# Kernel tuning notes

Measured on AMD Instinct MI355X. Metric: run time of the kernel, lower is better.

Reference implementation:

```python
import jax, jax.numpy as jnp
import numpy as np

B, IN, OUT, COND, N, H = 512, 256, 256, 128, 8, 64
DP = max(1, int(OUT * 0.25))          # 64 periodic units (cos+sin -> 2*DP outputs)
DN = OUT - 2 * DP                     # 128 non-periodic units
TPE = IN * DP + IN * DN + DN          # params per expert
TOTAL = N * TPE


def setup_inputs() -> dict:
    key = jax.random.key(0)
    ks = jax.random.split(key, 16)
    s_in = np.sqrt(2.0 / IN).astype(np.float32)
    inp = {
        "x": jax.random.normal(ks[0], (B, IN), jnp.float32),
        "cond": jax.random.normal(ks[1], (B, COND), jnp.float32),
        # expert base weights (torch: randn * sqrt(2/in))
        "base_wp": jax.random.normal(ks[2], (N, IN, DP), jnp.float32) * s_in,
        "base_wn": jax.random.normal(ks[3], (N, IN, DN), jnp.float32) * s_in,
        "base_bn": jnp.zeros((N, DN), jnp.float32),
        # hypernet: Linear(cond,H) -> ReLU -> Linear(H, TOTAL)
        "hW1": jax.random.normal(ks[4], (COND, H), jnp.float32) / np.sqrt(COND),
        "hb1": jnp.zeros((H,), jnp.float32),
        "hW2": jax.random.normal(ks[5], (H, TOTAL), jnp.float32) / np.sqrt(H),
        "hb2": jnp.zeros((TOTAL,), jnp.float32),
        # gating: Linear(cond,3N) -> ReLU -> Linear(3N, N)
        "gW1": jax.random.normal(ks[6], (COND, 3 * N), jnp.float32) / np.sqrt(COND),
        "gb1": jnp.zeros((3 * N,), jnp.float32),
        "gW2": jax.random.normal(ks[7], (3 * N, N), jnp.float32) / np.sqrt(3 * N),
        "gb2": jnp.zeros((N,), jnp.float32),
    }
    return inp


def reference(x, cond, base_wp, base_wn, base_bn,
              hW1, hb1, hW2, hb2, gW1, gb1, gW2, gb2):
    bsz = x.shape[0]
    # hypernet -> per-sample dynamic deltas
    h = jax.nn.relu(cond @ hW1 + hb1)
    delta = (h @ hW2 + hb2).reshape(bsz, N, TPE)
    d_wp = delta[:, :, : IN * DP].reshape(bsz, N, IN, DP)
    d_wn = delta[:, :, IN * DP: IN * DP + IN * DN].reshape(bsz, N, IN, DN)
    d_bn = delta[:, :, IN * DP + IN * DN:]                  # (B, N, DN)

    # periodic branch: per-sample, per-expert mat-vec then cos/sin
    wp = base_wp[None] + d_wp                                # (B,N,IN,DP)
    per = jnp.einsum('bi,bnip->bnp', x, wp)                  # (B,N,DP)
    per_cos, per_sin = jnp.cos(per), jnp.sin(per)

    # non-periodic branch
    wn = base_wn[None] + d_wn                                # (B,N,IN,DN)
    non = jnp.einsum('bi,bnip->bnp', x, wn) + base_bn[None] + d_bn
    non = jax.nn.relu(non)                                   # (B,N,DN)

    # gating over experts
    logits = jax.nn.relu(cond @ gW1 + gb1) @ gW2 + gb2       # (B,N)
    gw = jax.nn.softmax(logits, axis=1)[:, :, None]          # (B,N,1)

    cos_c = jnp.sum(per_cos * gw, axis=1)
    sin_c = jnp.sum(per_sin * gw, axis=1)
    non_c = jnp.sum(non * gw, axis=1)
    return jnp.concatenate([cos_c, sin_c, non_c], axis=-1)   # (B, 2*DP+DN)
```

## Files before the change

kernel.cpp:

```cpp
#include <hip/hip_runtime.h>
#include <math.h>

#define BB     512
#define INF    256
#define CONDF  128
#define NEXP   8
#define HDIM   64
#define TPE    49280
#define TOTC   394240
#define NSPLIT 16
#define CW     1536
#define KB     261

#define AZ_OFF 0u
#define BT_OFF 17104896u
#define P_OFF  68419584u
#define GW_OFF 93585408u
#define CB_OFF 93601792u

typedef __bf16          bf16x8 __attribute__((ext_vector_type(8)));
typedef unsigned short  us8    __attribute__((ext_vector_type(8)));
typedef float           f32x4  __attribute__((ext_vector_type(4)));

__device__ __forceinline__ unsigned short f2bf(float f) {
  unsigned u = __builtin_bit_cast(unsigned, f);
  u += 0x7fffu + ((u >> 16) & 1u);
  return (unsigned short)(u >> 16);
}
__device__ __forceinline__ float bf2f(unsigned short u) {
  return __builtin_bit_cast(float, ((unsigned)u) << 16);
}

__device__ __forceinline__ void gld16(const void* g, const void* l) {
  __builtin_amdgcn_global_load_lds(
      (const __attribute__((address_space(1))) unsigned int*)g,
      (__attribute__((address_space(3))) unsigned int*)l, 16, 0, 0);
}

__global__ __launch_bounds__(256, 4)
void k_bt(const float* __restrict__ hW2, unsigned short* __restrict__ Bt,
          const float* __restrict__ bwp, const float* __restrict__ bwn,
          const float* __restrict__ bbn, const float* __restrict__ hb2,
          float* __restrict__ colbias,
          const float* __restrict__ x, const float* __restrict__ cond,
          const float* __restrict__ hW1, const float* __restrict__ hb1,
          const float* __restrict__ gW1, const float* __restrict__ gb1,
          const float* __restrict__ gW2, const float* __restrict__ gb2,
          unsigned short* __restrict__ Az, float* __restrict__ gw) {
  const int bx = blockIdx.x;
  const int tid = threadIdx.x;
  __shared__ __align__(16) unsigned short Ls[64 * 256];

  if (bx >= 2072) {
    const int ne = bx - 2072;
    unsigned short* L2 = Ls;
#pragma unroll
    for (int it = 0; it < 8; ++it) {
      const int f = it * 256 + tid;
      const int t = f >> 5, c4 = (f & 31) * 4;
      f32x4 v = *(const f32x4*)(hW2 + (size_t)t * TOTC + (size_t)ne * TPE + 49152 + c4);
#pragma unroll
      for (int j = 0; j < 4; ++j) L2[t * 129 + c4 + j] = f2bf(v[j]);
    }
    if (tid < 192)
      colbias[ne * 192 + tid] = (tid < 64) ? 0.f
        : bbn[ne * 128 + (tid - 64)] + hb2[(size_t)ne * TPE + 49152 + (tid - 64)];
    __syncthreads();
    if (tid < 128) {
      const int c = tid;
#pragma unroll
      for (int t8 = 0; t8 < 8; ++t8) {
        us8 o;
#pragma unroll
        for (int j = 0; j < 8; ++j) o[j] = L2[(t8 * 8 + j) * 129 + c];
        *(us8*)(Bt + ((size_t)260 * CW + ne * 192 + 64 + c) * 64 + t8 * 8) = o;
      }
    } else {
      const int cz = (tid - 128) >> 1, hf = (tid - 128) & 1;
      us8 z = (us8){0, 0, 0, 0, 0, 0, 0, 0};
#pragma unroll
      for (int t8 = 0; t8 < 4; ++t8)
        *(us8*)(Bt + ((size_t)260 * CW + ne * 192 + cz) * 64 + (hf * 4 + t8) * 8) = z;
    }
    return;
  }

  if (bx >= 1536 && bx < 2048) {
    const int b = bx - 1536;
    float* xs  = (float*)Ls;
    float* cs  = xs + INF;
    float* hs  = cs + CONDF;
    float* g1  = hs + HDIM;
    float* lsb = g1 + 24;
    float* es  = lsb + 8;
    xs[tid] = x[b * INF + tid];
    if (tid < CONDF) cs[tid] = cond[b * CONDF + tid];
    __syncthreads();
    if (tid < HDIM) {
      float acc = hb1[tid];
      for (int q = 0; q < CONDF; ++q) acc = fmaf(cs[q], hW1[q * HDIM + tid], acc);
      hs[tid] = fmaxf(acc, 0.f);
    }
    if (tid >= 64 && tid < 88) {
      const int r = tid - 64;
      float acc = gb1[r];
      for (int q = 0; q < CONDF; ++q) acc = fmaf(cs[q], gW1[q * 24 + r], acc);
      g1[r] = fmaxf(acc, 0.f);
    }
    __syncthreads();
    if (tid < NEXP) {
      float acc = gb2[tid];
      for (int j = 0; j < 24; ++j) acc = fmaf(g1[j], gW2[j * NEXP + tid], acc);
      lsb[tid] = acc;
    }
    __syncthreads();
    if (tid < NEXP) {
      float m = lsb[0];
      for (int j = 1; j < NEXP; ++j) m = fmaxf(m, lsb[j]);
      es[tid] = expf(lsb[tid] - m);
    }
    __syncthreads();
    if (tid < NEXP) {
      float s = 0.f;
      for (int j = 0; j < NEXP; ++j) s += es[j];
      gw[b * NEXP + tid] = es[tid] / s;
    }
    const int t0 = tid >> 5, ig = tid & 31;
#pragma unroll
    for (int tt = 0; tt < 8; ++tt) {
      const int t = tt * 8 + t0;
      const float hv = hs[t];
      us8 o;
#pragma unroll
      for (int j = 0; j < 8; ++j) o[j] = f2bf(hv * xs[ig * 8 + j]);
      *(us8*)(Az + ((size_t)(t * 4 + (ig >> 3)) * BB + b) * 64 + (ig & 7) * 8) = o;
    }
    Az[((size_t)(256 + (tid >> 6)) * BB + b) * 64 + (tid & 63)] = f2bf(xs[tid]);
    if (tid < HDIM) Az[((size_t)260 * BB + b) * 64 + tid] = f2bf(hs[tid]);
    return;
  }

  const int pq = tid & 15, rg = tid >> 4, p4 = pq * 4;
  int kbBase, cbase;

  if (bx < 1536) {
    const int t = bx / 24, rem = bx % 24, ne = rem / 3, sec = rem % 3;
    const int dst  = sec ? 128 : 64;
    const int poff = (sec == 2) ? 64 : 0;
    kbBase = t * 4;
    cbase  = ne * 192 + sec * 64;
    const float* src = hW2 + (size_t)t * TOTC + (size_t)ne * TPE
                       + (sec ? 16384 : 0) + poff + p4;
    f32x4 va[8], vb[8];
#pragma unroll
    for (int it = 0; it < 8; ++it) {
      const int i0 = rg * 2 + it * 32;
      va[it] = *(const f32x4*)(src + (size_t)i0 * dst);
      vb[it] = *(const f32x4*)(src + (size_t)(i0 + 1) * dst);
    }
#pragma unroll
    for (int it = 0; it < 8; ++it) {
      const int i0 = rg * 2 + it * 32;
      const int e = i0 >> 3, q0 = i0 & 7;
#pragma unroll
      for (int j = 0; j < 4; ++j) {
        const int p = p4 + j;
        const unsigned lo = f2bf(va[it][j]), hi = f2bf(vb[it][j]);
        *(unsigned*)(&Ls[(p << 8) + (((e ^ (p >> 2)) << 3) | q0)]) = lo | (hi << 16);
      }
    }
  } else {
    const int u = bx - 2048, ne = u / 3, sec = u % 3;
    const int dst  = sec ? 128 : 64;
    const int poff = (sec == 2) ? 64 : 0;
    kbBase = 256;
    cbase  = ne * 192 + sec * 64;
    const float* s1 = sec ? (bwn + (size_t)ne * INF * 128 + poff)
                          : (bwp + (size_t)ne * INF * 64);
    const float* s2 = hb2 + (size_t)ne * TPE + (sec ? 16384 : 0) + poff;
#pragma unroll
    for (int it = 0; it < 8; ++it) {
      const int i0 = rg * 2 + it * 32;
      f32x4 a1 = *(const f32x4*)(s1 + (size_t)i0 * dst + p4);
      f32x4 a2 = *(const f32x4*)(s2 + (size_t)i0 * dst + p4);
      f32x4 b1 = *(const f32x4*)(s1 + (size_t)(i0 + 1) * dst + p4);
      f32x4 b2 = *(const f32x4*)(s2 + (size_t)(i0 + 1) * dst + p4);
      const int e = i0 >> 3, q0 = i0 & 7;
#pragma unroll
      for (int j = 0; j < 4; ++j) {
        const int p = p4 + j;
        const unsigned lo = f2bf(a1[j] + a2[j]);
        const unsigned hi = f2bf(b1[j] + b2[j]);
        *(unsigned*)(&Ls[(p << 8) + (((e ^ (p >> 2)) << 3) | q0)]) = lo | (hi << 16);
      }
    }
  }
  __syncthreads();
  us8 o[8];
#pragma unroll
  for (int it2 = 0; it2 < 8; ++it2) {
    const int of = it2 * 256 + tid;
    const int p = of >> 5, seg = of & 31;
    o[it2] = *(const us8*)(&Ls[(p << 8) + ((seg ^ (p >> 2)) << 3)]);
  }
#pragma unroll
  for (int it2 = 0; it2 < 8; ++it2) {
    const int of = it2 * 256 + tid;
    const int p = of >> 5, seg = of & 31, ib = seg >> 3, k8 = seg & 7;
    *(us8*)(Bt + ((size_t)(kbBase + ib) * CW + cbase + p) * 64 + k8 * 8) = o[it2];
  }
}

__launch_bounds__(256, 3)
__global__ void k_gemm(const unsigned short* __restrict__ Az,
                       const unsigned short* __restrict__ Bt,
                       unsigned short* __restrict__ P) {
  const int bid = blockIdx.x;
  const int g  = (bid >> 5) * 8 + (bid & 7);
  const int mt = (bid >> 3) & 3;
  const int nt = g >> 4;
  const int s  = g & 15;
  const int m0 = mt * 128, n0 = nt * 128;
  const int kb0 = s * 16 + (s < 5 ? s : 5);
  const int kb1 = kb0 + 16 + (s < 5 ? 1 : 0);
  const int tid = threadIdx.x;
  __shared__ __align__(16) unsigned short As[128 * 64];
  __shared__ __align__(16) unsigned short Bs[128 * 64];

  f32x4 acc[4][4];
#pragma unroll
  for (int mi = 0; mi < 4; ++mi)
#pragma unroll
    for (int ni = 0; ni < 4; ++ni) acc[mi][ni] = (f32x4){0.f, 0.f, 0.f, 0.f};

  const int wv = tid >> 6, lane = tid & 63;
  const int wm = wv >> 1, wn = wv & 1;
  const int lrow = lane & 15, quad = lane >> 4;
  const int srow = tid >> 3;
  const int sg0  = tid & 7;

  const unsigned short* ab = Az + ((size_t)kb0 * BB + m0) * 64;
  const unsigned short* bb = Bt + ((size_t)kb0 * CW + n0) * 64;

  for (int kb = kb0; kb < kb1; ++kb) {
#pragma unroll
    for (int it = 0; it < 4; ++it) {
      const int r = it * 32 + srow;
      const int ga = sg0 ^ (r & 7);
      const int ldsoff = __builtin_amdgcn_readfirstlane(it * 4096 + wv * 1024);
      gld16(ab + (size_t)r * 64 + ga * 8, (const char*)As + ldsoff);
      gld16(bb + (size_t)r * 64 + ga * 8, (const char*)Bs + ldsoff);
    }
    __syncthreads();
#pragma unroll
    for (int kh = 0; kh < 2; ++kh) {
      bf16x8 af[4], bfr[4];
#pragma unroll
      for (int mi = 0; mi < 4; ++mi) {
        const int r = wm * 64 + mi * 16 + lrow;
        const int ga = (kh * 4 + quad) ^ (r & 7);
        af[mi] = *(const bf16x8*)(As + r * 64 + ga * 8);
      }
#pragma unroll
      for (int ni = 0; ni < 4; ++ni) {
        const int r = wn * 64 + ni * 16 + lrow;
        const int ga = (kh * 4 + quad) ^ (r & 7);
        bfr[ni] = *(const bf16x8*)(Bs + r * 64 + ga * 8);
      }
#pragma unroll
      for (int mi = 0; mi < 4; ++mi)
#pragma unroll
        for (int ni = 0; ni < 4; ++ni)
          acc[mi][ni] = __builtin_amdgcn_mfma_f32_16x16x32_bf16(af[mi], bfr[ni], acc[mi][ni], 0, 0, 0);
    }
    __syncthreads();
    ab += (size_t)BB * 64;
    bb += (size_t)CW * 64;
  }

#pragma unroll
  for (int mi = 0; mi < 4; ++mi) {
    const int row0 = m0 + wm * 64 + mi * 16 + quad * 4;
#pragma unroll
    for (int ni = 0; ni < 4; ++ni) {
      const int col = n0 + wn * 64 + ni * 16 + lrow;
      unsigned short* pp = P + ((size_t)s * BB + row0) * CW + col;
#pragma unroll
      for (int r = 0; r < 4; ++r) pp[(size_t)r * CW] = f2bf(acc[mi][ni][r]);
    }
  }
}

__global__ void k_epi(const unsigned short* __restrict__ P, const float* __restrict__ gw,
                      const float* __restrict__ colbias, float* __restrict__ out) {
  const int b = blockIdx.x;
  const int r = threadIdx.x;
  __shared__ float gws[NEXP];
  if (r < NEXP) gws[r] = gw[b * NEXP + r];
  __syncthreads();
  float co = 0.f, si = 0.f, nc = 0.f;
  for (int n = 0; n < NEXP; ++n) {
    const int c = n * 192 + r;
    float v = colbias[c];
#pragma unroll
    for (int s2 = 0; s2 < NSPLIT; ++s2) v += bf2f(P[((size_t)s2 * BB + b) * CW + c]);
    const float g = gws[n];
    if (r < 64) { co = fmaf(g, cosf(v), co); si = fmaf(g, sinf(v), si); }
    else        { nc = fmaf(g, fmaxf(v, 0.f), nc); }
  }
  if (r < 64) { out[b * 256 + r] = co; out[b * 256 + 64 + r] = si; }
  else        { out[b * 256 + 128 + (r - 64)] = nc; }
}

extern "C" void kernel_launch(void* const* d_in, const int* in_sizes, int n_in,
                              void* d_out, int out_size, void* d_ws, size_t ws_size,
                              hipStream_t stream) {
  const float* x    = (const float*)d_in[0];
  const float* cond = (const float*)d_in[1];
  const float* bwp  = (const float*)d_in[2];
  const float* bwn  = (const float*)d_in[3];
  const float* bbn  = (const float*)d_in[4];
  const float* hW1  = (const float*)d_in[5];
  const float* hb1  = (const float*)d_in[6];
  const float* hW2  = (const float*)d_in[7];
  const float* hb2  = (const float*)d_in[8];
  const float* gW1  = (const float*)d_in[9];
  const float* gb1  = (const float*)d_in[10];
  const float* gW2  = (const float*)d_in[11];
  const float* gb2  = (const float*)d_in[12];
  float* out = (float*)d_out;
  char* ws = (char*)d_ws;

  unsigned short* Az = (unsigned short*)(ws + AZ_OFF);
  unsigned short* Bt = (unsigned short*)(ws + BT_OFF);
  unsigned short* Pp = (unsigned short*)(ws + P_OFF);
  float* gw      = (float*)(ws + GW_OFF);
  float* colbias = (float*)(ws + CB_OFF);

  hipLaunchKernelGGL(k_bt, dim3(2080), dim3(256), 0, stream,
                     hW2, Bt, bwp, bwn, bbn, hb2, colbias,
                     x, cond, hW1, hb1, gW1, gb1, gW2, gb2, Az, gw);
  hipLaunchKernelGGL(k_gemm, dim3(768), dim3(256), 0, stream, Az, Bt, Pp);
  hipLaunchKernelGGL(k_epi, dim3(BB), dim3(192), 0, stream, Pp, gw, colbias, out);
}
```

Measured before the change: 215.0 us.

## Fuse hW2 fp32-to-bf16 transpose into GEMM B-tile loads, drop Bt staging buffer

The main hypernet weight slab (hW2) is no longer converted to a bf16 transposed Bt buffer in a separate prep kernel. The GEMM now reads fp32 hW2 directly for k-blocks below 256, converts to bf16 and writes the swizzled B tile into LDS. Only the small base-weight and bias k-blocks still go through a prep buffer. This removes a large write and re-read of about 50 MB of bf16 data, in exchange for synchronous fp32 register loads and conversion in the GEMM inner loop instead of async global_load_lds, which may expose load latency.

```diff
diff --git a/kernel.cpp b/kernel.cpp
--- a/kernel.cpp
+++ b/kernel.cpp
@@ -12,11 +12,11 @@
 #define CW     1536
 #define KB     261
 
-#define AZ_OFF 0u
-#define BT_OFF 17104896u
-#define P_OFF  68419584u
-#define GW_OFF 93585408u
-#define CB_OFF 93601792u
+#define AZ_OFF  0u
+#define BTS_OFF 17104896u
+#define P_OFF   18087936u
+#define GW_OFF  43253760u
+#define CB_OFF  43270144u
 
 typedef __bf16          bf16x8 __attribute__((ext_vector_type(8)));
 typedef unsigned short  us8    __attribute__((ext_vector_type(8)));
@@ -38,55 +38,21 @@
 }
 
 __global__ __launch_bounds__(256, 4)
-void k_bt(const float* __restrict__ hW2, unsigned short* __restrict__ Bt,
-          const float* __restrict__ bwp, const float* __restrict__ bwn,
-          const float* __restrict__ bbn, const float* __restrict__ hb2,
-          float* __restrict__ colbias,
-          const float* __restrict__ x, const float* __restrict__ cond,
-          const float* __restrict__ hW1, const float* __restrict__ hb1,
-          const float* __restrict__ gW1, const float* __restrict__ gb1,
-          const float* __restrict__ gW2, const float* __restrict__ gb2,
-          unsigned short* __restrict__ Az, float* __restrict__ gw) {
+void k_prep(const float* __restrict__ hW2, unsigned short* __restrict__ Bts,
+            const float* __restrict__ bwp, const float* __restrict__ bwn,
+            const float* __restrict__ bbn, const float* __restrict__ hb2,
+            float* __restrict__ colbias,
+            const float* __restrict__ x, const float* __restrict__ cond,
+            const float* __restrict__ hW1, const float* __restrict__ hb1,
+            const float* __restrict__ gW1, const float* __restrict__ gb1,
+            const float* __restrict__ gW2, const float* __restrict__ gb2,
+            unsigned short* __restrict__ Az, float* __restrict__ gw) {
   const int bx = blockIdx.x;
   const int tid = threadIdx.x;
   __shared__ __align__(16) unsigned short Ls[64 * 256];
 
-  if (bx >= 2072) {
-    const int ne = bx - 2072;
-    unsigned short* L2 = Ls;
-#pragma unroll
-    for (int it = 0; it < 8; ++it) {
-      const int f = it * 256 + tid;
-      const int t = f >> 5, c4 = (f & 31) * 4;
-      f32x4 v = *(const f32x4*)(hW2 + (size_t)t * TOTC + (size_t)ne * TPE + 49152 + c4);
-#pragma unroll
-      for (int j = 0; j < 4; ++j) L2[t * 129 + c4 + j] = f2bf(v[j]);
-    }
-    if (tid < 192)
-      colbias[ne * 192 + tid] = (tid < 64) ? 0.f
-        : bbn[ne * 128 + (tid - 64)] + hb2[(size_t)ne * TPE + 49152 + (tid - 64)];
-    __syncthreads();
-    if (tid < 128) {
-      const int c = tid;
-#pragma unroll
-      for (int t8 = 0; t8 < 8; ++t8) {
-        us8 o;
-#pragma unroll
-        for (int j = 0; j < 8; ++j) o[j] = L2[(t8 * 8 + j) * 129 + c];
-        *(us8*)(Bt + ((size_t)260 * CW + ne * 192 + 64 + c) * 64 + t8 * 8) = o;
-      }
-    } else {
-      const int cz = (tid - 128) >> 1, hf = (tid - 128) & 1;
-      us8 z = (us8){0, 0, 0, 0, 0, 0, 0, 0};
-#pragma unroll
-      for (int t8 = 0; t8 < 4; ++t8)
-        *(us8*)(Bt + ((size_t)260 * CW + ne * 192 + cz) * 64 + (hf * 4 + t8) * 8) = z;
-    }
-    return;
-  }
-
-  if (bx >= 1536 && bx < 2048) {
-    const int b = bx - 1536;
+  if (bx < 512) {
+    const int b = bx;
     float* xs  = (float*)Ls;
     float* cs  = xs + INF;
     float* hs  = cs + CONDF;
@@ -140,59 +106,62 @@
     return;
   }
 
+  if (bx >= 536) {
+    const int ne = bx - 536;
+    unsigned short* L2 = Ls;
+#pragma unroll
+    for (int it = 0; it < 8; ++it) {
+      const int f = it * 256 + tid;
+      const int t = f >> 5, c4 = (f & 31) * 4;
+      f32x4 v = *(const f32x4*)(hW2 + (size_t)t * TOTC + (size_t)ne * TPE + 49152 + c4);
+#pragma unroll
+      for (int j = 0; j < 4; ++j) L2[t * 129 + c4 + j] = f2bf(v[j]);
+    }
+    if (tid < 192)
+      colbias[ne * 192 + tid] = (tid < 64) ? 0.f
+        : bbn[ne * 128 + (tid - 64)] + hb2[(size_t)ne * TPE + 49152 + (tid - 64)];
+    __syncthreads();
+    if (tid < 128) {
+      const int c = tid;
+#pragma unroll
+      for (int t8 = 0; t8 < 8; ++t8) {
+        us8 o;
+#pragma unroll
+        for (int j = 0; j < 8; ++j) o[j] = L2[(t8 * 8 + j) * 129 + c];
+        *(us8*)(Bts + ((size_t)4 * CW + ne * 192 + 64 + c) * 64 + t8 * 8) = o;
+      }
+    } else {
+      const int cz = (tid - 128) >> 1, hf = (tid - 128) & 1;
+      us8 z = (us8){0, 0, 0, 0, 0, 0, 0, 0};
+#pragma unroll
+      for (int t8 = 0; t8 < 4; ++t8)
+        *(us8*)(Bts + ((size_t)4 * CW + ne * 192 + cz) * 64 + (hf * 4 + t8) * 8) = z;
+    }
+    return;
+  }
+
   const int pq = tid & 15, rg = tid >> 4, p4 = pq * 4;
-  int kbBase, cbase;
-
-  if (bx < 1536) {
-    const int t = bx / 24, rem = bx % 24, ne = rem / 3, sec = rem % 3;
-    const int dst  = sec ? 128 : 64;
-    const int poff = (sec == 2) ? 64 : 0;
-    kbBase = t * 4;
-    cbase  = ne * 192 + sec * 64;
-    const float* src = hW2 + (size_t)t * TOTC + (size_t)ne * TPE
-                       + (sec ? 16384 : 0) + poff + p4;
-    f32x4 va[8], vb[8];
-#pragma unroll
-    for (int it = 0; it < 8; ++it) {
-      const int i0 = rg * 2 + it * 32;
-      va[it] = *(const f32x4*)(src + (size_t)i0 * dst);
-      vb[it] = *(const f32x4*)(src + (size_t)(i0 + 1) * dst);
-    }
-#pragma unroll
-    for (int it = 0; it < 8; ++it) {
-      const int i0 = rg * 2 + it * 32;
-      const int e = i0 >> 3, q0 = i0 & 7;
-#pragma unroll
-      for (int j = 0; j < 4; ++j) {
-        const int p = p4 + j;
-        const unsigned lo = f2bf(va[it][j]), hi = f2bf(vb[it][j]);
-        *(unsigned*)(&Ls[(p << 8) + (((e ^ (p >> 2)) << 3) | q0)]) = lo | (hi << 16);
-      }
-    }
-  } else {
-    const int u = bx - 2048, ne = u / 3, sec = u % 3;
-    const int dst  = sec ? 128 : 64;
-    const int poff = (sec == 2) ? 64 : 0;
-    kbBase = 256;
-    cbase  = ne * 192 + sec * 64;
-    const float* s1 = sec ? (bwn + (size_t)ne * INF * 128 + poff)
-                          : (bwp + (size_t)ne * INF * 64);
-    const float* s2 = hb2 + (size_t)ne * TPE + (sec ? 16384 : 0) + poff;
-#pragma unroll
-    for (int it = 0; it < 8; ++it) {
-      const int i0 = rg * 2 + it * 32;
-      f32x4 a1 = *(const f32x4*)(s1 + (size_t)i0 * dst + p4);
-      f32x4 a2 = *(const f32x4*)(s2 + (size_t)i0 * dst + p4);
-      f32x4 b1 = *(const f32x4*)(s1 + (size_t)(i0 + 1) * dst + p4);
-      f32x4 b2 = *(const f32x4*)(s2 + (size_t)(i0 + 1) * dst + p4);
-      const int e = i0 >> 3, q0 = i0 & 7;
-#pragma unroll
-      for (int j = 0; j < 4; ++j) {
-        const int p = p4 + j;
-        const unsigned lo = f2bf(a1[j] + a2[j]);
-        const unsigned hi = f2bf(b1[j] + b2[j]);
-        *(unsigned*)(&Ls[(p << 8) + (((e ^ (p >> 2)) << 3) | q0)]) = lo | (hi << 16);
-      }
+  const int u = bx - 512, ne = u / 3, sec = u % 3;
+  const int dst  = sec ? 128 : 64;
+  const int poff = (sec == 2) ? 64 : 0;
+  const int cbase = ne * 192 + sec * 64;
+  const float* s1 = sec ? (bwn + (size_t)ne * INF * 128 + poff)
+                        : (bwp + (size_t)ne * INF * 64);
+  const float* s2 = hb2 + (size_t)ne * TPE + (sec ? 16384 : 0) + poff;
+#pragma unroll
+  for (int it = 0; it < 8; ++it) {
+    const int i0 = rg * 2 + it * 32;
+    f32x4 a1 = *(const f32x4*)(s1 + (size_t)i0 * dst + p4);
+    f32x4 a2 = *(const f32x4*)(s2 + (size_t)i0 * dst + p4);
+    f32x4 b1 = *(const f32x4*)(s1 + (size_t)(i0 + 1) * dst + p4);
+    f32x4 b2 = *(const f32x4*)(s2 + (size_t)(i0 + 1) * dst + p4);
+    const int e = i0 >> 3, q0 = i0 & 7;
+#pragma unroll
+    for (int j = 0; j < 4; ++j) {
+      const int p = p4 + j;
+      const unsigned lo = f2bf(a1[j] + a2[j]);
+      const unsigned hi = f2bf(b1[j] + b2[j]);
+      *(unsigned*)(&Ls[(p << 8) + (((e ^ (p >> 2)) << 3) | q0)]) = lo | (hi << 16);
     }
   }
   __syncthreads();
@@ -207,13 +176,14 @@
   for (int it2 = 0; it2 < 8; ++it2) {
     const int of = it2 * 256 + tid;
     const int p = of >> 5, seg = of & 31, ib = seg >> 3, k8 = seg & 7;
-    *(us8*)(Bt + ((size_t)(kbBase + ib) * CW + cbase + p) * 64 + k8 * 8) = o[it2];
+    *(us8*)(Bts + ((size_t)ib * CW + cbase + p) * 64 + k8 * 8) = o[it2];
   }
 }
 
 __launch_bounds__(256, 3)
 __global__ void k_gemm(const unsigned short* __restrict__ Az,
-                       const unsigned short* __restrict__ Bt,
+                       const float* __restrict__ hW2,
+                       const unsigned short* __restrict__ Bts,
                        unsigned short* __restrict__ P) {
   const int bid = blockIdx.x;
   const int g  = (bid >> 5) * 8 + (bid & 7);
@@ -239,17 +209,56 @@
   const int srow = tid >> 3;
   const int sg0  = tid & 7;
 
-  const unsigned short* ab = Az + ((size_t)kb0 * BB + m0) * 64;
-  const unsigned short* bb = Bt + ((size_t)kb0 * CW + n0) * 64;
+  const int half = tid >> 7;
+  const int mq   = (tid >> 3) & 15;
+  const int pi   = tid & 7;
+  const int ch   = n0 + half * 64;
+  const int neb  = ch / 192;
+  const int r0   = ch - neb * 192;
+  const int wp   = (r0 < 64);
+  const int sh   = wp ? 6 : 7;
+  const float* Bh = hW2 + (size_t)(neb * TPE + (wp ? r0 : 16384 + (r0 - 64)) + mq * 4);
+  const int rbase = half * 64 + mq * 4;
 
   for (int kb = kb0; kb < kb1; ++kb) {
+    const unsigned short* ab = Az + ((size_t)kb * BB + m0) * 64;
 #pragma unroll
     for (int it = 0; it < 4; ++it) {
       const int r = it * 32 + srow;
       const int ga = sg0 ^ (r & 7);
       const int ldsoff = __builtin_amdgcn_readfirstlane(it * 4096 + wv * 1024);
       gld16(ab + (size_t)r * 64 + ga * 8, (const char*)As + ldsoff);
-      gld16(bb + (size_t)r * 64 + ga * 8, (const char*)Bs + ldsoff);
+    }
+    if (kb < 256) {
+      const float* Br = Bh + (size_t)(kb >> 2) * TOTC;
+      const int i0 = (kb & 3) * 64;
+      f32x4 va[4], vb[4];
+#pragma unroll
+      for (int it = 0; it < 4; ++it) {
+        const int ko = pi * 2 + it * 16;
+        va[it] = *(const f32x4*)(Br + ((i0 + ko) << sh));
+        vb[it] = *(const f32x4*)(Br + ((i0 + ko + 1) << sh));
+      }
+#pragma unroll
+      for (int it = 0; it < 4; ++it) {
+        const int gg = (pi >> 2) + it * 2;
+#pragma unroll
+        for (int j = 0; j < 4; ++j) {
+          const int rl = rbase + j;
+          const unsigned lo = f2bf(va[it][j]), hi = f2bf(vb[it][j]);
+          *(unsigned*)((char*)Bs + rl * 128 + ((gg ^ (rl & 7)) << 4) + ((pi & 3) << 2))
+              = lo | (hi << 16);
+        }
+      }
+    } else {
+      const unsigned short* bbp = Bts + ((size_t)(kb - 256) * CW + n0) * 64;
+#pragma unroll
+      for (int it = 0; it < 4; ++it) {
+        const int r = it * 32 + srow;
+        const int ga = sg0 ^ (r & 7);
+        const int ldsoff = __builtin_amdgcn_readfirstlane(it * 4096 + wv * 1024);
+        gld16(bbp + (size_t)r * 64 + ga * 8, (const char*)Bs + ldsoff);
+      }
     }
     __syncthreads();
 #pragma unroll
@@ -274,8 +283,6 @@
           acc[mi][ni] = __builtin_amdgcn_mfma_f32_16x16x32_bf16(af[mi], bfr[ni], acc[mi][ni], 0, 0, 0);
     }
     __syncthreads();
-    ab += (size_t)BB * 64;
-    bb += (size_t)CW * 64;
   }
 
 #pragma unroll
@@ -331,15 +338,15 @@
   float* out = (float*)d_out;
   char* ws = (char*)d_ws;
 
-  unsigned short* Az = (unsigned short*)(ws + AZ_OFF);
-  unsigned short* Bt = (unsigned short*)(ws + BT_OFF);
-  unsigned short* Pp = (unsigned short*)(ws + P_OFF);
+  unsigned short* Az  = (unsigned short*)(ws + AZ_OFF);
+  unsigned short* Bts = (unsigned short*)(ws + BTS_OFF);
+  unsigned short* Pp  = (unsigned short*)(ws + P_OFF);
   float* gw      = (float*)(ws + GW_OFF);
   float* colbias = (float*)(ws + CB_OFF);
 
-  hipLaunchKernelGGL(k_bt, dim3(2080), dim3(256), 0, stream,
-                     hW2, Bt, bwp, bwn, bbn, hb2, colbias,
+  hipLaunchKernelGGL(k_prep, dim3(544), dim3(256), 0, stream,
+                     hW2, Bts, bwp, bwn, bbn, hb2, colbias,
                      x, cond, hW1, hb1, gW1, gb1, gW2, gb2, Az, gw);
-  hipLaunchKernelGGL(k_gemm, dim3(768), dim3(256), 0, stream, Az, Bt, Pp);
+  hipLaunchKernelGGL(k_gemm, dim3(768), dim3(256), 0, stream, Az, hW2, Bts, Pp);
   hipLaunchKernelGGL(k_epi, dim3(BB), dim3(192), 0, stream, Pp, gw, colbias, out);
 }
```

After: 236.6 us. 10.0% more time.
